# Kernel tuning notes

Measured on AMD Instinct MI355X. Metric: run time of the kernel, lower is better.

The kernel has to match this reference:

```python
import jax, jax.numpy as jnp
import numpy as np

EPS = 1e-5

def setup_inputs() -> dict:
    key = jax.random.key(0)
    ks = jax.random.split(key, 5)
    B, C, N, L = 32, 128, 4096, 6
    M = N // 8  # 512
    x = jax.random.normal(ks[0], (B, C, N, 1), dtype=jnp.float32)
    # small init scale keeps softmax logits in a sane range
    W_pool = jax.random.normal(ks[1], (M, C), dtype=jnp.float32) * 0.05
    Wf = jax.random.normal(ks[2], (L, M, M), dtype=jnp.float32) * 0.02
    gamma = jnp.ones((L, M), dtype=jnp.float32)
    beta = jnp.zeros((L, M), dtype=jnp.float32)
    W_unpool = jax.random.normal(ks[3], (M, C), dtype=jnp.float32) * 0.05
    b_unpool = jnp.zeros((M,), dtype=jnp.float32)
    return {"x": x, "W_pool": W_pool, "Wf": Wf, "gamma": gamma,
            "beta": beta, "W_unpool": W_unpool, "b_unpool": b_unpool}


def reference(x, W_pool, Wf, gamma, beta, W_unpool, b_unpool):
    # x: [B, C, N, 1]
    xs = x[..., 0]  # [B, C, N]
    # ---- Pool_1_to_1: 1x1 conv C->M, softmax over N, weighted sum ----
    Spool = jax.nn.softmax(jnp.einsum('mc,bcn->bmn', W_pool, xs), axis=2)
    h = jnp.einsum('bcn,bmn->bmc', xs, Spool)  # pooled then transposed: [B, M, C]
    # ---- n_layers of Order_Aware_Filtering_1_to_1 on [B, M, C] (channels=M) ----
    L = Wf.shape[0]
    for l in range(L):
        y = jnp.einsum('om,bmc->boc', Wf[l], h)  # 1x1 conv M->M
        mu = jnp.mean(y, axis=(0, 2), keepdims=True)          # BN over (B, spatial)
        var = jnp.mean((y - mu) ** 2, axis=(0, 2), keepdims=True)  # biased var
        yn = (y - mu) * jax.lax.rsqrt(var + EPS)
        yn = yn * gamma[l][None, :, None] + beta[l][None, :, None]
        h = jax.nn.relu(yn + h)  # residual + non-lin
    x1 = jnp.transpose(h, (0, 2, 1))  # [B, C, M]
    # ---- Unpool_1_to_1: 1x1 conv (with bias) C->M, softmax over M ----
    ul = jnp.einsum('mc,bcn->bmn', W_unpool, xs) + b_unpool[None, :, None]
    Sun = jax.nn.softmax(ul, axis=1)
    out = jnp.einsum('bcm,bmn->bcn', x1, Sun)
    return out[..., None]  # [B, C, N, 1]
```

## Files before the change

### kernel.cpp

```cpp
#include <hip/hip_runtime.h>
#include <hip/hip_bf16.h>

typedef float f32x4 __attribute__((ext_vector_type(4)));
typedef __bf16 bf16_t;
typedef __bf16 bf16x4 __attribute__((ext_vector_type(4)));
typedef __bf16 bf16x8 __attribute__((ext_vector_type(8)));

#define MFMA16(a, b, c) __builtin_amdgcn_mfma_f32_16x16x32_bf16(a, b, c, 0, 0, 0)

constexpr int C_ = 128;
constexpr int N_ = 4096;
constexpr int M_ = 512;
constexpr int NL = 6;

#define NEG_INF (-__builtin_huge_valf())

constexpr int XST = 136;
constexpr int NSTP = 40;
constexpr int PSTU = 72;

__global__ __launch_bounds__(256) void k_wsplit(const float* __restrict__ W,
                                                bf16_t* __restrict__ hi,
                                                bf16_t* __restrict__ lo) {
  const size_t i4 = ((size_t)blockIdx.x * 256 + threadIdx.x) * 4;
  f32x4 v = *(const f32x4*)&W[i4];
  bf16x4 h4, l4;
#pragma unroll
  for (int k = 0; k < 4; ++k) {
    bf16_t h = (bf16_t)v[k];
    h4[k] = h;
    l4[k] = (bf16_t)(v[k] - (float)h);
  }
  *(bf16x4*)&hi[i4] = h4;
  *(bf16x4*)&lo[i4] = l4;
}

__global__ __launch_bounds__(256) void k_xsplit(const float* __restrict__ xs,
                                                bf16_t* __restrict__ thi,
                                                bf16_t* __restrict__ tlo) {
  __shared__ float T[128 * 68];
  const int n0 = blockIdx.x * 64, b = blockIdx.y;
  const int t = threadIdx.x;
  const float* xsb = xs + (size_t)b * C_ * N_;
#pragma unroll
  for (int i = 0; i < 8; ++i) {
    int slot = i * 256 + t;
    int c = slot >> 4, n4 = (slot & 15) * 4;
    *(f32x4*)&T[c * 68 + n4] = *(const f32x4*)&xsb[(size_t)c * N_ + n0 + n4];
  }
  __syncthreads();
  const int n = t >> 2, cb = (t & 3) * 32;
  bf16x8 h8[4], l8[4];
#pragma unroll
  for (int g = 0; g < 4; ++g)
#pragma unroll
    for (int j = 0; j < 8; ++j) {
      float v = T[(cb + g * 8 + j) * 68 + n];
      bf16_t hh = (bf16_t)v;
      h8[g][j] = hh;
      l8[g][j] = (bf16_t)(v - (float)hh);
    }
  const size_t base = ((size_t)b * N_ + n0 + n) * C_ + cb;
#pragma unroll
  for (int g = 0; g < 4; ++g) {
    *(bf16x8*)&thi[base + g * 8] = h8[g];
    *(bf16x8*)&tlo[base + g * 8] = l8[g];
  }
}

__global__ __launch_bounds__(256) void k_pool(const bf16_t* __restrict__ xsThi,
                                              const bf16_t* __restrict__ xsTlo,
                                              const float* __restrict__ x,
                                              const bf16_t* __restrict__ Wph,
                                              const bf16_t* __restrict__ Wpl,
                                              float* __restrict__ h_part,
                                              float* __restrict__ ml) {
  __shared__ bf16_t XH[32 * XST], XL[32 * XST];
  __shared__ bf16_t XCH[128 * NSTP], XCL[128 * NSTP];
  const int d = blockIdx.x;
  const int lin = ((d & 7) << 7) | (d >> 3);
  const int b = lin >> 5, r5 = lin & 31;
  const int mt = r5 >> 2, seg = r5 & 3;
  const int m0 = mt * 64;
  const int t = threadIdx.x, w = t >> 6, lane = t & 63, l15 = lane & 15, q = lane >> 4;

  const int sn0 = t >> 4, sn1 = (256 + t) >> 4;
  const int scg = (t & 15) * 8;
  const size_t sgb = ((size_t)b * N_ + seg * 1024) * C_ + scg;
  const int xc = t >> 3, xn4 = (t & 7) * 4;
  const float* xb = x + (size_t)b * C_ * N_;

  bf16x8 aWh[4], aWl[4];
#pragma unroll
  for (int k = 0; k < 4; ++k) {
    const size_t ra = (size_t)(m0 + w * 16 + l15) * C_ + k * 32 + q * 8;
    aWh[k] = *(const bf16x8*)&Wph[ra];
    aWl[k] = *(const bf16x8*)&Wpl[ra];
  }

  f32x4 acc[8];
#pragma unroll
  for (int cs = 0; cs < 8; ++cs) acc[cs] = f32x4{0.f, 0.f, 0.f, 0.f};
  float lsum = 0.f;

  for (int ch = 0; ch < 32; ++ch) {
    const int n0g = seg * 1024 + ch * 32;
    const size_t off = sgb + (size_t)ch * 32 * C_;
    __syncthreads();
    bf16x8 th0 = *(const bf16x8*)&xsThi[off + (size_t)sn0 * C_];
    bf16x8 th1 = *(const bf16x8*)&xsThi[off + (size_t)sn1 * C_];
    bf16x8 tl0 = *(const bf16x8*)&xsTlo[off + (size_t)sn0 * C_];
    bf16x8 tl1 = *(const bf16x8*)&xsTlo[off + (size_t)sn1 * C_];
    f32x4 xv[4];
#pragma unroll
    for (int i = 0; i < 4; ++i) {
      const int c = xc + i * 32;
      xv[i] = *(const f32x4*)&xb[(size_t)c * N_ + n0g + xn4];
    }
    *(bf16x8*)&XH[sn0 * XST + scg] = th0;
    *(bf16x8*)&XH[sn1 * XST + scg] = th1;
    *(bf16x8*)&XL[sn0 * XST + scg] = tl0;
    *(bf16x8*)&XL[sn1 * XST + scg] = tl1;
#pragma unroll
    for (int i = 0; i < 4; ++i) {
      const int c = xc + i * 32;
      bf16x4 h4, l4;
#pragma unroll
      for (int j = 0; j < 4; ++j) {
        bf16_t hh = (bf16_t)xv[i][j];
        h4[j] = hh;
        l4[j] = (bf16_t)(xv[i][j] - (float)hh);
      }
      *(bf16x4*)&XCH[c * NSTP + xn4] = h4;
      *(bf16x4*)&XCL[c * NSTP + xn4] = l4;
    }
    __syncthreads();

    f32x4 U0 = f32x4{0.f, 0.f, 0.f, 0.f}, U1 = f32x4{0.f, 0.f, 0.f, 0.f};
#pragma unroll
    for (int k = 0; k < 4; ++k) {
      {
        const int o = l15 * XST + k * 32 + q * 8;
        bf16x8 bh = *(const bf16x8*)&XH[o];
        bf16x8 bl = *(const bf16x8*)&XL[o];
        U0 = MFMA16(bh, aWh[k], U0);
        U0 = MFMA16(bl, aWh[k], U0);
        U0 = MFMA16(bh, aWl[k], U0);
      }
      {
        const int o = (16 + l15) * XST + k * 32 + q * 8;
        bf16x8 bh = *(const bf16x8*)&XH[o];
        bf16x8 bl = *(const bf16x8*)&XL[o];
        U1 = MFMA16(bh, aWh[k], U1);
        U1 = MFMA16(bl, aWh[k], U1);
        U1 = MFMA16(bh, aWl[k], U1);
      }
    }

    f32x4 pe0, pe1;
#pragma unroll
    for (int r = 0; r < 4; ++r) {
      pe0[r] = __expf(U0[r]);
      pe1[r] = __expf(U1[r]);
      lsum += pe0[r] + pe1[r];
    }

    const int slo = l15 + ((lane & 16) ? 32 : 0);
    float pj[8];
#pragma unroll
    for (int r = 0; r < 4; ++r) {
      float a0 = __shfl(pe0[r], slo);
      float a1 = __shfl(pe1[r], slo);
      pj[r] = (q & 2) ? a1 : a0;
      float b0 = __shfl(pe0[r], slo + 16);
      float b1 = __shfl(pe1[r], slo + 16);
      pj[4 + r] = (q & 2) ? b1 : b0;
    }
    bf16x8 aPh, aPl;
#pragma unroll
    for (int j = 0; j < 8; ++j) {
      bf16_t hh = (bf16_t)pj[j];
      aPh[j] = hh;
      aPl[j] = (bf16_t)(pj[j] - (float)hh);
    }

#pragma unroll
    for (int cs = 0; cs < 8; ++cs) {
      const int ob = (cs * 16 + l15) * NSTP + q * 8;
      bf16x8 bh = *(const bf16x8*)&XCH[ob];
      bf16x8 bl = *(const bf16x8*)&XCL[ob];
      acc[cs] = MFMA16(aPh, bh, acc[cs]);
      acc[cs] = MFMA16(aPh, bl, acc[cs]);
      acc[cs] = MFMA16(aPl, bh, acc[cs]);
    }
  }

  const size_t sb = (size_t)seg * 32 + b;
  lsum += __shfl_xor(lsum, 16);
  lsum += __shfl_xor(lsum, 32);
  if (lane < 16) ml[sb * 512 + m0 + w * 16 + lane] = lsum;
#pragma unroll
  for (int cs = 0; cs < 8; ++cs)
#pragma unroll
    for (int r = 0; r < 4; ++r) {
      const int m = m0 + w * 16 + q * 4 + r;
      h_part[(sb * 512 + m) * 128 + cs * 16 + l15] = acc[cs][r];
    }
}

__global__ __launch_bounds__(128) void k_combine(const float* __restrict__ h_part,
                                                 const float* __restrict__ ml,
                                                 float* __restrict__ hbuf) {
  const int mb = blockIdx.x;
  const int m = mb >> 5, b = mb & 31;
  const int c = threadIdx.x;
  float L = 0.f, acc = 0.f;
#pragma unroll
  for (int s = 0; s < 4; ++s) {
    L += ml[((size_t)s * 32 + b) * 512 + m];
    acc += h_part[(((size_t)s * 32 + b) * 512 + m) * 128 + c];
  }
  hbuf[(size_t)m * 4096 + b * 128 + c] = acc / L;
}

__global__ __launch_bounds__(256) void k_hsplit(const float* __restrict__ h,
                                                bf16_t* __restrict__ thi,
                                                bf16_t* __restrict__ tlo) {
  __shared__ float T[64 * 65];
  const int m0 = blockIdx.x * 64, c0 = blockIdx.y * 64;
  const int t = threadIdx.x;
#pragma unroll
  for (int ii = 0; ii < 4; ++ii) {
    int slot = ii * 256 + t;
    int m = slot >> 4, c4 = (slot & 15) * 4;
    f32x4 v = *(const f32x4*)&h[(size_t)(m0 + m) * 4096 + c0 + c4];
#pragma unroll
    for (int k = 0; k < 4; ++k) T[(c4 + k) * 65 + m] = v[k];
  }
  __syncthreads();
  const int row = t >> 2, mg = (t & 3) * 16;
  bf16x8 h8[2], l8[2];
#pragma unroll
  for (int half = 0; half < 2; ++half)
#pragma unroll
    for (int j = 0; j < 8; ++j) {
      float v = T[row * 65 + mg + half * 8 + j];
      bf16_t hh = (bf16_t)v;
      h8[half][j] = hh;
      l8[half][j] = (bf16_t)(v - (float)hh);
    }
  bf16_t* ph = &thi[(size_t)(c0 + row) * 512 + m0 + mg];
  bf16_t* pl = &tlo[(size_t)(c0 + row) * 512 + m0 + mg];
  *(bf16x8*)ph = h8[0];
  *(bf16x8*)(ph + 8) = h8[1];
  *(bf16x8*)pl = l8[0];
  *(bf16x8*)(pl + 8) = l8[1];
}

__global__ __launch_bounds__(256) void k_bnsplit(const float* __restrict__ ybuf,
                                                 float* __restrict__ hbuf,
                                                 const float* __restrict__ stats,
                                                 const float* __restrict__ gamma,
                                                 const float* __restrict__ beta,
                                                 int l,
                                                 bf16_t* __restrict__ thi,
                                                 bf16_t* __restrict__ tlo) {
  __shared__ float T[64 * 65];
  const int m0 = blockIdx.x * 64, c0 = blockIdx.y * 64;
  const int t = threadIdx.x;
#pragma unroll
  for (int ii = 0; ii < 4; ++ii) {
    int slot = ii * 256 + t;
    int m = slot >> 4, c4 = (slot & 15) * 4;
    const int o = m0 + m;
    const float mu = stats[l * 1024 + o] * (1.f / 4096.f);
    const float var = stats[l * 1024 + 512 + o] * (1.f / 4096.f) - mu * mu;
    const float rs = rsqrtf(var + 1e-5f);
    const float g = gamma[l * 512 + o];
    const float bt = beta[l * 512 + o];
    const size_t gidx = (size_t)o * 4096 + c0 + c4;
    f32x4 y = *(const f32x4*)&ybuf[gidx];
    f32x4 h = *(const f32x4*)&hbuf[gidx];
    f32x4 r;
#pragma unroll
    for (int k = 0; k < 4; ++k) {
      r[k] = fmaxf((y[k] - mu) * rs * g + bt + h[k], 0.f);
      T[(c4 + k) * 65 + m] = r[k];
    }
    *(f32x4*)&hbuf[gidx] = r;
  }
  __syncthreads();
  const int row = t >> 2, mg = (t & 3) * 16;
  bf16x8 h8[2], l8[2];
#pragma unroll
  for (int half = 0; half < 2; ++half)
#pragma unroll
    for (int j = 0; j < 8; ++j) {
      float v = T[row * 65 + mg + half * 8 + j];
      bf16_t hh = (bf16_t)v;
      h8[half][j] = hh;
      l8[half][j] = (bf16_t)(v - (float)hh);
    }
  bf16_t* ph = &thi[(size_t)(c0 + row) * 512 + m0 + mg];
  bf16_t* pl = &tlo[(size_t)(c0 + row) * 512 + m0 + mg];
  *(bf16x8*)ph = h8[0];
  *(bf16x8*)(ph + 8) = h8[1];
  *(bf16x8*)pl = l8[0];
  *(bf16x8*)(pl + 8) = l8[1];
}

__global__ __launch_bounds__(256) void k_layerA(const bf16_t* __restrict__ Whi,
                                                const bf16_t* __restrict__ Wlo,
                                                const bf16_t* __restrict__ hThi,
                                                const bf16_t* __restrict__ hTlo,
                                                int l, float* __restrict__ ybuf,
                                                float* __restrict__ stats) {
  const int o0 = blockIdx.x * 32;
  const int bc0 = blockIdx.y * 128;
  const int t = threadIdx.x;
  const int w = t >> 6, lane = t & 63, l15 = lane & 15, q = lane >> 4;
  const int bcw = bc0 + w * 32;
  const bf16_t* Wh = Whi + (size_t)l * M_ * M_;
  const bf16_t* Wl = Wlo + (size_t)l * M_ * M_;

  f32x4 acc[2][2];
#pragma unroll
  for (int i = 0; i < 2; ++i)
#pragma unroll
    for (int j = 0; j < 2; ++j) acc[i][j] = f32x4{0.f, 0.f, 0.f, 0.f};

  for (int k0 = 0; k0 < M_; k0 += 32) {
    bf16x8 ah[2], al[2], bh[2], bl[2];
#pragma unroll
    for (int os = 0; os < 2; ++os) {
      const size_t ro = (size_t)(o0 + os * 16 + l15) * M_ + k0 + q * 8;
      ah[os] = *(const bf16x8*)&Wh[ro];
      al[os] = *(const bf16x8*)&Wl[ro];
    }
#pragma unroll
    for (int ns = 0; ns < 2; ++ns) {
      const size_t rb = (size_t)(bcw + ns * 16 + l15) * M_ + k0 + q * 8;
      bh[ns] = *(const bf16x8*)&hThi[rb];
      bl[ns] = *(const bf16x8*)&hTlo[rb];
    }
#pragma unroll
    for (int os = 0; os < 2; ++os)
#pragma unroll
      for (int ns = 0; ns < 2; ++ns) {
        acc[os][ns] = MFMA16(ah[os], bh[ns], acc[os][ns]);
        acc[os][ns] = MFMA16(ah[os], bl[ns], acc[os][ns]);
        acc[os][ns] = MFMA16(al[os], bh[ns], acc[os][ns]);
      }
  }

  float s1[2][4], s2[2][4];
#pragma unroll
  for (int os = 0; os < 2; ++os)
#pragma unroll
    for (int r = 0; r < 4; ++r) {
      float a = 0.f, b2 = 0.f;
#pragma unroll
      for (int ns = 0; ns < 2; ++ns) {
        float v = acc[os][ns][r];
        ybuf[(size_t)(o0 + os * 16 + q * 4 + r) * 4096 + bcw + ns * 16 + l15] = v;
        a += v;
        b2 += v * v;
      }
      s1[os][r] = a;
      s2[os][r] = b2;
    }
#pragma unroll
  for (int os = 0; os < 2; ++os)
#pragma unroll
    for (int r = 0; r < 4; ++r) {
#pragma unroll
      for (int off = 1; off < 16; off <<= 1) {
        s1[os][r] += __shfl_xor(s1[os][r], off);
        s2[os][r] += __shfl_xor(s2[os][r], off);
      }
      if (l15 == 0) {
        const int o = o0 + os * 16 + q * 4 + r;
        atomicAdd(&stats[l * 1024 + o], s1[os][r]);
        atomicAdd(&stats[l * 1024 + 512 + o], s2[os][r]);
      }
    }
}

__global__ __launch_bounds__(256) void k_unpool(const bf16_t* __restrict__ xsThi,
                                                const bf16_t* __restrict__ xsTlo,
                                                const bf16_t* __restrict__ Wuh,
                                                const bf16_t* __restrict__ Wul,
                                                const float* __restrict__ bun,
                                                const bf16_t* __restrict__ x1hi,
                                                const bf16_t* __restrict__ x1lo,
                                                float* __restrict__ out) {
  __shared__ bf16_t XH[64 * XST], XL[64 * XST];
  __shared__ bf16_t PH[64 * PSTU], PL[64 * PSTU];
  __shared__ float colsum_s[4][64];
  __shared__ float L_s[64];
  const int n0 = blockIdx.x * 64, b = blockIdx.y;
  const int t = threadIdx.x, w = t >> 6, lane = t & 63, l15 = lane & 15, q = lane >> 4;

#pragma unroll
  for (int i = 0; i < 4; ++i) {
    int slot = i * 256 + t;
    int n = slot >> 4, cg = (slot & 15) * 8;
    const size_t g = ((size_t)b * N_ + n0 + n) * C_ + cg;
    *(bf16x8*)&XH[n * XST + cg] = *(const bf16x8*)&xsThi[g];
    *(bf16x8*)&XL[n * XST + cg] = *(const bf16x8*)&xsTlo[g];
  }
  colsum_s[w][lane] = 0.f;
  f32x4 acc[2][4];
#pragma unroll
  for (int cs = 0; cs < 2; ++cs)
#pragma unroll
    for (int nt = 0; nt < 4; ++nt) acc[cs][nt] = f32x4{0.f, 0.f, 0.f, 0.f};
  __syncthreads();

  for (int ch = 0; ch < 8; ++ch) {
    const int mg0 = ch * 64 + w * 16;
    f32x4 U[4];
#pragma unroll
    for (int nt = 0; nt < 4; ++nt) U[nt] = f32x4{0.f, 0.f, 0.f, 0.f};
#pragma unroll
    for (int k = 0; k < 4; ++k) {
      const size_t ra = (size_t)(mg0 + l15) * C_ + k * 32 + q * 8;
      bf16x8 ah = *(const bf16x8*)&Wuh[ra];
      bf16x8 al = *(const bf16x8*)&Wul[ra];
#pragma unroll
      for (int nt = 0; nt < 4; ++nt) {
        const int o = (nt * 16 + l15) * XST + k * 32 + q * 8;
        bf16x8 bh = *(const bf16x8*)&XH[o];
        bf16x8 bl = *(const bf16x8*)&XL[o];
        U[nt] = MFMA16(ah, bh, U[nt]);
        U[nt] = MFMA16(ah, bl, U[nt]);
        U[nt] = MFMA16(al, bh, U[nt]);
      }
    }
    float bi[4];
#pragma unroll
    for (int r = 0; r < 4; ++r) bi[r] = bun[mg0 + q * 4 + r];

#pragma unroll
    for (int nt = 0; nt < 4; ++nt) {
      bf16x4 ph4, pl4;
      float s = 0.f;
#pragma unroll
      for (int r = 0; r < 4; ++r) {
        float pv = __expf(U[nt][r] + bi[r]);
        s += pv;
        bf16_t hh = (bf16_t)pv;
        ph4[r] = hh;
        pl4[r] = (bf16_t)(pv - (float)hh);
      }
      s += __shfl_xor(s, 16);
      s += __shfl_xor(s, 32);
      if (lane < 16) colsum_s[w][nt * 16 + lane] += s;
      const int o = (nt * 16 + l15) * PSTU + w * 16 + q * 4;
      *(bf16x4*)&PH[o] = ph4;
      *(bf16x4*)&PL[o] = pl4;
    }
    __syncthreads();

#pragma unroll
    for (int ks = 0; ks < 2; ++ks) {
      bf16x8 ah2[2], al2[2];
#pragma unroll
      for (int cs = 0; cs < 2; ++cs) {
        const size_t ga =
            ((size_t)b * 128 + w * 32 + cs * 16 + l15) * M_ + ch * 64 + ks * 32 + q * 8;
        ah2[cs] = *(const bf16x8*)&x1hi[ga];
        al2[cs] = *(const bf16x8*)&x1lo[ga];
      }
#pragma unroll
      for (int nt = 0; nt < 4; ++nt) {
        const int o = (nt * 16 + l15) * PSTU + ks * 32 + q * 8;
        bf16x8 bh = *(const bf16x8*)&PH[o];
        bf16x8 bl = *(const bf16x8*)&PL[o];
#pragma unroll
        for (int cs = 0; cs < 2; ++cs) {
          acc[cs][nt] = MFMA16(ah2[cs], bh, acc[cs][nt]);
          acc[cs][nt] = MFMA16(ah2[cs], bl, acc[cs][nt]);
          acc[cs][nt] = MFMA16(al2[cs], bh, acc[cs][nt]);
        }
      }
    }
    __syncthreads();
  }
  if (t < 64)
    L_s[t] = colsum_s[0][t] + colsum_s[1][t] + colsum_s[2][t] + colsum_s[3][t];
  __syncthreads();
#pragma unroll
  for (int nt = 0; nt < 4; ++nt) {
    const float invL = 1.f / L_s[nt * 16 + l15];
#pragma unroll
    for (int cs = 0; cs < 2; ++cs) {
      const int c = w * 32 + cs * 16 + q * 4;
#pragma unroll
      for (int r = 0; r < 4; ++r)
        out[((size_t)b * 128 + c + r) * (size_t)N_ + n0 + nt * 16 + l15] =
            acc[cs][nt][r] * invL;
    }
  }
}

extern "C" void kernel_launch(void* const* d_in, const int* in_sizes, int n_in,
                              void* d_out, int out_size, void* d_ws, size_t ws_size,
                              hipStream_t stream) {
  const float* x = (const float*)d_in[0];
  const float* W_pool = (const float*)d_in[1];
  const float* Wf = (const float*)d_in[2];
  const float* gamma = (const float*)d_in[3];
  const float* beta = (const float*)d_in[4];
  const float* W_unpool = (const float*)d_in[5];
  const float* b_unpool = (const float*)d_in[6];
  float* out = (float*)d_out;

  char* ws = (char*)d_ws;
  float* h_part = (float*)ws; ws += (size_t)4 * 32 * 512 * 128 * 4;
  float* ml = (float*)ws;     ws += (size_t)4 * 32 * 512 * 4;
  float* hbuf = (float*)ws;   ws += (size_t)512 * 4096 * 4;
  float* stats = (float*)ws;  ws += NL * 1024 * 4;
  bf16_t* xsThi = (bf16_t*)ws; ws += (size_t)32 * N_ * C_ * 2;
  bf16_t* xsTlo = (bf16_t*)ws; ws += (size_t)32 * N_ * C_ * 2;
  bf16_t* Wuh = (bf16_t*)ws;  ws += (size_t)M_ * C_ * 2;
  bf16_t* Wul = (bf16_t*)ws;  ws += (size_t)M_ * C_ * 2;
  bf16_t* Wph = (bf16_t*)ws;  ws += (size_t)M_ * C_ * 2;
  bf16_t* Wpl = (bf16_t*)ws;  ws += (size_t)M_ * C_ * 2;
  bf16_t* Whi = (bf16_t*)ws;  ws += (size_t)NL * M_ * M_ * 2;
  bf16_t* Wlo = (bf16_t*)ws;  ws += (size_t)NL * M_ * M_ * 2;
  char* hp = (char*)h_part;
  float* ybuf = (float*)(hp);
  bf16_t* hThi = (bf16_t*)(hp + 8388608);
  bf16_t* hTlo = (bf16_t*)(hp + 12582912);

  hipMemsetAsync(stats, 0, NL * 1024 * 4, stream);
  k_xsplit<<<dim3(64, 32), 256, 0, stream>>>(x, xsThi, xsTlo);
  k_wsplit<<<dim3(64), 256, 0, stream>>>(W_pool, Wph, Wpl);
  k_wsplit<<<dim3(64), 256, 0, stream>>>(W_unpool, Wuh, Wul);
  k_wsplit<<<dim3(1536), 256, 0, stream>>>(Wf, Whi, Wlo);
  k_pool<<<dim3(1024), 256, 0, stream>>>(xsThi, xsTlo, x, Wph, Wpl,
                                         h_part, ml);
  k_combine<<<dim3(16384), 128, 0, stream>>>(h_part, ml, hbuf);
  k_hsplit<<<dim3(8, 64), 256, 0, stream>>>(hbuf, hThi, hTlo);
  for (int l = 0; l < NL; ++l) {
    k_layerA<<<dim3(16, 32), 256, 0, stream>>>(Whi, Wlo, hThi, hTlo, l, ybuf, stats);
    k_bnsplit<<<dim3(8, 64), 256, 0, stream>>>(ybuf, hbuf, stats, gamma, beta, l,
                                               hThi, hTlo);
  }
  k_unpool<<<dim3(64, 32), 256, 0, stream>>>(xsThi, xsTlo, Wuh, Wul, b_unpool,
                                             hThi, hTlo, out);
}
```

Before: 769.2 us.

## Give each wave its own n-slice in unpool, pass softmax via shuffles

```diff
diff --git a/kernel.cpp b/kernel.cpp
--- a/kernel.cpp
+++ b/kernel.cpp
@@ -17,7 +17,6 @@
 
 constexpr int XST = 136;
 constexpr int NSTP = 40;
-constexpr int PSTU = 72;
 
 __global__ __launch_bounds__(256) void k_wsplit(const float* __restrict__ W,
                                                 bf16_t* __restrict__ hi,
@@ -395,9 +394,6 @@
                                                 const bf16_t* __restrict__ x1lo,
                                                 float* __restrict__ out) {
   __shared__ bf16_t XH[64 * XST], XL[64 * XST];
-  __shared__ bf16_t PH[64 * PSTU], PL[64 * PSTU];
-  __shared__ float colsum_s[4][64];
-  __shared__ float L_s[64];
   const int n0 = blockIdx.x * 64, b = blockIdx.y;
   const int t = threadIdx.x, w = t >> 6, lane = t & 63, l15 = lane & 15, q = lane >> 4;
 
@@ -409,97 +405,95 @@
     *(bf16x8*)&XH[n * XST + cg] = *(const bf16x8*)&xsThi[g];
     *(bf16x8*)&XL[n * XST + cg] = *(const bf16x8*)&xsTlo[g];
   }
-  colsum_s[w][lane] = 0.f;
-  f32x4 acc[2][4];
-#pragma unroll
-  for (int cs = 0; cs < 2; ++cs)
-#pragma unroll
-    for (int nt = 0; nt < 4; ++nt) acc[cs][nt] = f32x4{0.f, 0.f, 0.f, 0.f};
   __syncthreads();
 
+  bf16x8 bXh[4], bXl[4];
+#pragma unroll
+  for (int k = 0; k < 4; ++k) {
+    const int o = (w * 16 + l15) * XST + k * 32 + q * 8;
+    bXh[k] = *(const bf16x8*)&XH[o];
+    bXl[k] = *(const bf16x8*)&XL[o];
+  }
+
+  f32x4 acc[8];
+#pragma unroll
+  for (int cs = 0; cs < 8; ++cs) acc[cs] = f32x4{0.f, 0.f, 0.f, 0.f};
+  float lsum = 0.f;
+
   for (int ch = 0; ch < 8; ++ch) {
-    const int mg0 = ch * 64 + w * 16;
+    const int mg0 = ch * 64;
     f32x4 U[4];
 #pragma unroll
-    for (int nt = 0; nt < 4; ++nt) U[nt] = f32x4{0.f, 0.f, 0.f, 0.f};
+    for (int mt = 0; mt < 4; ++mt) U[mt] = f32x4{0.f, 0.f, 0.f, 0.f};
 #pragma unroll
     for (int k = 0; k < 4; ++k) {
-      const size_t ra = (size_t)(mg0 + l15) * C_ + k * 32 + q * 8;
-      bf16x8 ah = *(const bf16x8*)&Wuh[ra];
-      bf16x8 al = *(const bf16x8*)&Wul[ra];
-#pragma unroll
-      for (int nt = 0; nt < 4; ++nt) {
-        const int o = (nt * 16 + l15) * XST + k * 32 + q * 8;
-        bf16x8 bh = *(const bf16x8*)&XH[o];
-        bf16x8 bl = *(const bf16x8*)&XL[o];
-        U[nt] = MFMA16(ah, bh, U[nt]);
-        U[nt] = MFMA16(ah, bl, U[nt]);
-        U[nt] = MFMA16(al, bh, U[nt]);
-      }
-    }
-    float bi[4];
-#pragma unroll
-    for (int r = 0; r < 4; ++r) bi[r] = bun[mg0 + q * 4 + r];
-
-#pragma unroll
-    for (int nt = 0; nt < 4; ++nt) {
-      bf16x4 ph4, pl4;
-      float s = 0.f;
+#pragma unroll
+      for (int mt = 0; mt < 4; ++mt) {
+        const size_t ra = (size_t)(mg0 + mt * 16 + l15) * C_ + k * 32 + q * 8;
+        bf16x8 ah = *(const bf16x8*)&Wuh[ra];
+        bf16x8 al = *(const bf16x8*)&Wul[ra];
+        U[mt] = MFMA16(ah, bXh[k], U[mt]);
+        U[mt] = MFMA16(ah, bXl[k], U[mt]);
+        U[mt] = MFMA16(al, bXh[k], U[mt]);
+      }
+    }
+
+    f32x4 pe[4];
+#pragma unroll
+    for (int mt = 0; mt < 4; ++mt) {
+      f32x4 bi = *(const f32x4*)&bun[mg0 + mt * 16 + q * 4];
 #pragma unroll
       for (int r = 0; r < 4; ++r) {
-        float pv = __expf(U[nt][r] + bi[r]);
-        s += pv;
-        bf16_t hh = (bf16_t)pv;
-        ph4[r] = hh;
-        pl4[r] = (bf16_t)(pv - (float)hh);
-      }
-      s += __shfl_xor(s, 16);
-      s += __shfl_xor(s, 32);
-      if (lane < 16) colsum_s[w][nt * 16 + lane] += s;
-      const int o = (nt * 16 + l15) * PSTU + w * 16 + q * 4;
-      *(bf16x4*)&PH[o] = ph4;
-      *(bf16x4*)&PL[o] = pl4;
-    }
-    __syncthreads();
-
+        float pv = __expf(U[mt][r] + bi[r]);
+        pe[mt][r] = pv;
+        lsum += pv;
+      }
+    }
+
+    const int slo = l15 + ((lane & 16) ? 32 : 0);
 #pragma unroll
     for (int ks = 0; ks < 2; ++ks) {
-      bf16x8 ah2[2], al2[2];
-#pragma unroll
-      for (int cs = 0; cs < 2; ++cs) {
+      float pj[8];
+#pragma unroll
+      for (int r = 0; r < 4; ++r) {
+        float a0 = __shfl(pe[2 * ks][r], slo);
+        float a1 = __shfl(pe[2 * ks + 1][r], slo);
+        pj[r] = (q & 2) ? a1 : a0;
+        float b0 = __shfl(pe[2 * ks][r], slo + 16);
+        float b1 = __shfl(pe[2 * ks + 1][r], slo + 16);
+        pj[4 + r] = (q & 2) ? b1 : b0;
+      }
+      bf16x8 bPh, bPl;
+#pragma unroll
+      for (int j = 0; j < 8; ++j) {
+        bf16_t hh = (bf16_t)pj[j];
+        bPh[j] = hh;
+        bPl[j] = (bf16_t)(pj[j] - (float)hh);
+      }
+#pragma unroll
+      for (int cs = 0; cs < 8; ++cs) {
         const size_t ga =
-            ((size_t)b * 128 + w * 32 + cs * 16 + l15) * M_ + ch * 64 + ks * 32 + q * 8;
-        ah2[cs] = *(const bf16x8*)&x1hi[ga];
-        al2[cs] = *(const bf16x8*)&x1lo[ga];
-      }
-#pragma unroll
-      for (int nt = 0; nt < 4; ++nt) {
-        const int o = (nt * 16 + l15) * PSTU + ks * 32 + q * 8;
-        bf16x8 bh = *(const bf16x8*)&PH[o];
-        bf16x8 bl = *(const bf16x8*)&PL[o];
-#pragma unroll
-        for (int cs = 0; cs < 2; ++cs) {
-          acc[cs][nt] = MFMA16(ah2[cs], bh, acc[cs][nt]);
-          acc[cs][nt] = MFMA16(ah2[cs], bl, acc[cs][nt]);
-          acc[cs][nt] = MFMA16(al2[cs], bh, acc[cs][nt]);
-        }
-      }
-    }
-    __syncthreads();
-  }
-  if (t < 64)
-    L_s[t] = colsum_s[0][t] + colsum_s[1][t] + colsum_s[2][t] + colsum_s[3][t];
-  __syncthreads();
-#pragma unroll
-  for (int nt = 0; nt < 4; ++nt) {
-    const float invL = 1.f / L_s[nt * 16 + l15];
-#pragma unroll
-    for (int cs = 0; cs < 2; ++cs) {
-      const int c = w * 32 + cs * 16 + q * 4;
-#pragma unroll
-      for (int r = 0; r < 4; ++r)
-        out[((size_t)b * 128 + c + r) * (size_t)N_ + n0 + nt * 16 + l15] =
-            acc[cs][nt][r] * invL;
+            ((size_t)b * 128 + cs * 16 + l15) * M_ + mg0 + ks * 32 + q * 8;
+        bf16x8 ah = *(const bf16x8*)&x1hi[ga];
+        bf16x8 al = *(const bf16x8*)&x1lo[ga];
+        acc[cs] = MFMA16(ah, bPh, acc[cs]);
+        acc[cs] = MFMA16(ah, bPl, acc[cs]);
+        acc[cs] = MFMA16(al, bPh, acc[cs]);
+      }
+    }
+  }
+
+  lsum += __shfl_xor(lsum, 16);
+  lsum += __shfl_xor(lsum, 32);
+  const float invL = 1.f / lsum;
+
+#pragma unroll
+  for (int cs = 0; cs < 8; ++cs) {
+#pragma unroll
+    for (int r = 0; r < 4; ++r) {
+      const int c = cs * 16 + q * 4 + r;
+      out[((size_t)b * 128 + c) * (size_t)N_ + n0 + w * 16 + l15] =
+          acc[cs][r] * invL;
     }
   }
 }
```

Result: slower. 1.077 ms (+40.0%).
